# Kernel tuning notes

Hardware: AMD Instinct MI355X
Metric: run time of the kernel (lower is better)

## Reference

```python
import jax, jax.numpy as jnp
import numpy as np

EPS = 1e-6
NUM_HEADS = 16


def _layernorm(x, g, b):
    m = jnp.mean(x, axis=-1, keepdims=True)
    v = jnp.mean(jnp.square(x - m), axis=-1, keepdims=True)
    return (x - m) / jnp.sqrt(v + EPS) * g + b


def _rotate_half(x):
    x1, x2 = jnp.split(x, 2, axis=-1)
    return jnp.concatenate([-x2, x1], axis=-1)


def setup_inputs() -> dict:
    key = jax.random.key(0)
    B, N, C = 2, 2048, 1024
    H = NUM_HEADS
    D = C // H
    F = int(C * 4.0)
    ks = jax.random.split(key, 12)
    s = 0.02
    pos = jnp.arange(N)[:, None].astype(jnp.float32)
    inv_freq = 1.0 / (10000.0 ** (jnp.arange(0, D, 2, dtype=jnp.float32) / D))
    freqs = pos * inv_freq[None, :]          # [N, D/2]
    emb = jnp.concatenate([freqs, freqs], axis=-1)  # [N, D]
    return {
        "x": jax.random.normal(ks[0], (B, N, C), jnp.float32),
        "rotary_cos": jnp.cos(emb),
        "rotary_sin": jnp.sin(emb),
        "ln1_g": jnp.ones((C,), jnp.float32),
        "ln1_b": jnp.zeros((C,), jnp.float32),
        "Wq": jax.random.normal(ks[1], (C, C), jnp.float32) * s,
        "bq": jnp.zeros((C,), jnp.float32),
        "Wk": jax.random.normal(ks[2], (C, C), jnp.float32) * s,
        "bk": jnp.zeros((C,), jnp.float32),
        "Wv": jax.random.normal(ks[3], (C, C), jnp.float32) * s,
        "bv": jnp.zeros((C,), jnp.float32),
        "Wo": jax.random.normal(ks[4], (C, C), jnp.float32) * s,
        "bo": jnp.zeros((C,), jnp.float32),
        "ln2_g": jnp.ones((C,), jnp.float32),
        "ln2_b": jnp.zeros((C,), jnp.float32),
        "W1": jax.random.normal(ks[5], (F, C), jnp.float32) * s,
        "b1": jnp.zeros((F,), jnp.float32),
        "W2": jax.random.normal(ks[6], (C, F), jnp.float32) * s,
        "b2": jnp.zeros((C,), jnp.float32),
    }


def reference(x, rotary_cos, rotary_sin, ln1_g, ln1_b, Wq, bq, Wk, bk, Wv, bv,
              Wo, bo, ln2_g, ln2_b, W1, b1, W2, b2):
    B, N, C = x.shape
    H = NUM_HEADS
    D = C // H

    # --- attention branch ---
    h = _layernorm(x, ln1_g, ln1_b)
    q = (h @ Wq.T + bq).reshape(B, N, H, D).transpose(0, 2, 1, 3)  # [B,H,N,D]
    k = (h @ Wk.T + bk).reshape(B, N, H, D).transpose(0, 2, 1, 3)
    v = (h @ Wv.T + bv).reshape(B, N, H, D).transpose(0, 2, 1, 3)

    cos = rotary_cos[None, None, :, :]  # [1,1,N,D]
    sin = rotary_sin[None, None, :, :]
    q = q * cos + _rotate_half(q) * sin
    k = k * cos + _rotate_half(k) * sin

    scale = D ** -0.5
    attn = jnp.einsum('bhnd,bhmd->bhnm', q, k) * scale
    attn = jax.nn.softmax(attn, axis=-1)
    out = jnp.einsum('bhnm,bhmd->bhnd', attn, v)
    out = out.transpose(0, 2, 1, 3).reshape(B, N, C)
    out = out @ Wo.T + bo
    x = x + out

    # --- MLP branch ---
    h = _layernorm(x, ln2_g, ln2_b)
    h = jax.nn.gelu(h @ W1.T + b1, approximate=False)  # torch nn.GELU exact
    h = h @ W2.T + b2
    return x + h
```

## Files before the change

kernel.cpp:

```cpp
#include <hip/hip_runtime.h>
#include <hip/hip_bf16.h>

#define B_ 2
#define N_ 2048
#define C_ 1024
#define H_ 16
#define D_ 64
#define F_ 4096
#define M_ 4096

typedef __attribute__((ext_vector_type(8))) short bf16x8;
typedef __attribute__((ext_vector_type(4))) float f32x4;

__device__ inline unsigned short f2bf(float f) {
  unsigned int u = __float_as_uint(f);
  u = (u + 0x7FFFu + ((u >> 16) & 1u)) >> 16;
  return (unsigned short)u;
}

__global__ __launch_bounds__(256)
void cvt_all(const float4* __restrict__ s0, const float4* __restrict__ s1,
             const float4* __restrict__ s2, const float4* __restrict__ s3,
             const float4* __restrict__ s4, const float4* __restrict__ s5,
             ushort4* __restrict__ d0, ushort4* __restrict__ d1,
             ushort4* __restrict__ d2, ushort4* __restrict__ d3,
             ushort4* __restrict__ d4, ushort4* __restrict__ d5) {
  int b = blockIdx.x;
  const float4* s; ushort4* d; int i;
  if      (b < 1024) { s = s0; d = d0; i = b * 256 + threadIdx.x; }
  else if (b < 2048) { s = s1; d = d1; i = (b - 1024) * 256 + threadIdx.x; }
  else if (b < 3072) { s = s2; d = d2; i = (b - 2048) * 256 + threadIdx.x; }
  else if (b < 4096) { s = s3; d = d3; i = (b - 3072) * 256 + threadIdx.x; }
  else if (b < 8192) { s = s4; d = d4; i = (b - 4096) * 256 + threadIdx.x; }
  else               { s = s5; d = d5; i = (b - 8192) * 256 + threadIdx.x; }
  float4 f = s[i];
  ushort4 o;
  o.x = f2bf(f.x); o.y = f2bf(f.y); o.z = f2bf(f.z); o.w = f2bf(f.w);
  d[i] = o;
}

__global__ __launch_bounds__(256)
void ln_kernel(const float* __restrict__ x, const float* __restrict__ g,
               const float* __restrict__ b, unsigned short* __restrict__ out) {
  __shared__ float red[8];
  const int row = blockIdx.x;
  const int t = threadIdx.x;
  const float4 xv = *(const float4*)(x + row * 1024 + t * 4);
  float s  = xv.x + xv.y + xv.z + xv.w;
  float sq = xv.x * xv.x + xv.y * xv.y + xv.z * xv.z + xv.w * xv.w;
  #pragma unroll
  for (int off = 32; off >= 1; off >>= 1) {
    s  += __shfl_down(s, off);
    sq += __shfl_down(sq, off);
  }
  const int lane = t & 63, wave = t >> 6;
  if (lane == 0) { red[wave * 2] = s; red[wave * 2 + 1] = sq; }
  __syncthreads();
  float ts = red[0] + red[2] + red[4] + red[6];
  float tq = red[1] + red[3] + red[5] + red[7];
  float mean = ts * (1.0f / 1024.0f);
  float var  = tq * (1.0f / 1024.0f) - mean * mean;
  float rstd = rsqrtf(var + 1e-6f);
  float xs[4] = {xv.x, xv.y, xv.z, xv.w};
  #pragma unroll
  for (int i = 0; i < 4; i++) {
    int c = t * 4 + i;
    float y = (xs[i] - mean) * rstd * g[c] + b[c];
    out[row * 1024 + c] = f2bf(y);
  }
}

template<int MODE, int BN>
__global__ __launch_bounds__(256)
void gemm_bt(const unsigned short* __restrict__ A,
             const unsigned short* __restrict__ Bw,
             int K, int Nout, int npc,
             const float* __restrict__ bias,
             const float* __restrict__ resid,
             unsigned short* __restrict__ out_bf,
             float* __restrict__ out_f32) {
  constexpr int NJ = BN / 32;
  __shared__ unsigned short sA[2][128 * 64];
  __shared__ unsigned short sB[2][BN * 64];
  const int t = threadIdx.x;
  const int wave = t >> 6, lane = t & 63;
  const int quad = lane >> 4, l16 = lane & 15;
  const int wm = (wave & 1) * 64, wn = (wave >> 1) * (BN / 2);
  const int id = blockIdx.y * gridDim.x + blockIdx.x;
  const int xcd = id & 7, r_ = id >> 3;
  const int n_blk = xcd * npc + r_ % npc;
  const int m_blk = r_ / npc;
  const int m0 = m_blk * 128, n0 = n_blk * BN;

  f32x4 acc[4][NJ];
  #pragma unroll
  for (int i = 0; i < 4; i++)
    #pragma unroll
    for (int j = 0; j < NJ; j++) acc[i][j] = (f32x4){0.f, 0.f, 0.f, 0.f};

  const unsigned short* gA = A  + (m0 + (t >> 3)) * K + (t & 7) * 8;
  const unsigned short* gB = Bw + (n0 + (t >> 3)) * K + (t & 7) * 8;

  auto stage = [&](int k0, int buf) {
    unsigned short* lA = &sA[buf][(wave * 8) * 64];
    unsigned short* lB = &sB[buf][(wave * 8) * 64];
    #pragma unroll
    for (int i = 0; i < 4; i++)
      __builtin_amdgcn_global_load_lds((const unsigned int*)(gA + (32 * i) * K + k0),
                                       (unsigned int*)(lA + 32 * i * 64), 16, 0, 0);
    #pragma unroll
    for (int i = 0; i < BN / 32; i++)
      __builtin_amdgcn_global_load_lds((const unsigned int*)(gB + (32 * i) * K + k0),
                                       (unsigned int*)(lB + 32 * i * 64), 16, 0, 0);
  };

  stage(0, 0);
  __syncthreads();

  const int nk = K >> 6;
  for (int kt = 0; kt < nk; kt++) {
    const int cur = kt & 1;
    if (kt + 1 < nk) stage((kt + 1) * 64, cur ^ 1);
    #pragma unroll
    for (int kk = 0; kk < 2; kk++) {
      bf16x8 af[4], bfr[NJ];
      #pragma unroll
      for (int i = 0; i < 4; i++)
        af[i] = *(const bf16x8*)(&sA[cur][(wm + i * 16 + l16) * 64 + kk * 32 + quad * 8]);
      #pragma unroll
      for (int j = 0; j < NJ; j++)
        bfr[j] = *(const bf16x8*)(&sB[cur][(wn + j * 16 + l16) * 64 + kk * 32 + quad * 8]);
      #pragma unroll
      for (int i = 0; i < 4; i++)
        #pragma unroll
        for (int j = 0; j < NJ; j++)
          acc[i][j] = __builtin_amdgcn_mfma_f32_16x16x32_bf16(af[i], bfr[j], acc[i][j], 0, 0, 0);
    }
    __syncthreads();
  }

  #pragma unroll
  for (int i = 0; i < 4; i++) {
    #pragma unroll
    for (int j = 0; j < NJ; j++) {
      int col = n0 + wn + j * 16 + l16;
      #pragma unroll
      for (int r = 0; r < 4; r++) {
        int row = m0 + wm + i * 16 + quad * 4 + r;
        float v = acc[i][j][r];
        if (MODE == 1 || MODE == 3) {
          out_f32[row * Nout + col] = v + bias[col] + resid[row * Nout + col];
        } else {
          v += bias[col];
          float w = v * (1.0f + 0.044715f * v * v);
          float gl = v / (1.0f + __expf(-1.5957691216f * w));
          out_bf[row * Nout + col] = f2bf(gl);
        }
      }
    }
  }
}

__global__ __launch_bounds__(256)
void gemm_qkv(const unsigned short* __restrict__ A,
              const unsigned short* __restrict__ Bw,
              const float* __restrict__ bq, const float* __restrict__ bk,
              const float* __restrict__ bv,
              const float* __restrict__ rc, const float* __restrict__ rs,
              unsigned short* __restrict__ qo, unsigned short* __restrict__ ko,
              unsigned short* __restrict__ vt) {
  const int K = C_;
  __shared__ unsigned short sA[2][128 * 64];
  __shared__ unsigned short sB[2][128 * 64];
  const int t = threadIdx.x;
  const int wave = t >> 6, lane = t & 63;
  const int quad = lane >> 4, l16 = lane & 15;
  const int wm = (wave & 1) * 64, wn = (wave >> 1) * 64;
  const int id = blockIdx.y * gridDim.x + blockIdx.x;
  const int xcd = id & 7, r_ = id >> 3;
  const int n_blk = xcd * 3 + r_ % 3;
  const int m_blk = r_ / 3;
  const int m0 = m_blk * 128, n0 = n_blk * 128;

  f32x4 acc[4][4];
  #pragma unroll
  for (int i = 0; i < 4; i++)
    #pragma unroll
    for (int j = 0; j < 4; j++) acc[i][j] = (f32x4){0.f, 0.f, 0.f, 0.f};

  const unsigned short* gA = A  + (m0 + (t >> 3)) * K + (t & 7) * 8;
  const unsigned short* gB = Bw + (n0 + (t >> 3)) * K + (t & 7) * 8;

  auto stage = [&](int k0, int buf) {
    unsigned short* lA = &sA[buf][(wave * 8) * 64];
    unsigned short* lB = &sB[buf][(wave * 8) * 64];
    #pragma unroll
    for (int i = 0; i < 4; i++) {
      __builtin_amdgcn_global_load_lds((const unsigned int*)(gA + (32 * i) * K + k0),
                                       (unsigned int*)(lA + 32 * i * 64), 16, 0, 0);
      __builtin_amdgcn_global_load_lds((const unsigned int*)(gB + (32 * i) * K + k0),
                                       (unsigned int*)(lB + 32 * i * 64), 16, 0, 0);
    }
  };

  stage(0, 0);
  __syncthreads();

  const int nk = K >> 6;
  for (int kt = 0; kt < nk; kt++) {
    const int cur = kt & 1;
    if (kt + 1 < nk) stage((kt + 1) * 64, cur ^ 1);
    #pragma unroll
    for (int kk = 0; kk < 2; kk++) {
      bf16x8 af[4], bfr[4];
      #pragma unroll
      for (int i = 0; i < 4; i++)
        af[i] = *(const bf16x8*)(&sA[cur][(wm + i * 16 + l16) * 64 + kk * 32 + quad * 8]);
      #pragma unroll
      for (int j = 0; j < 4; j++)
        bfr[j] = *(const bf16x8*)(&sB[cur][(wn + j * 16 + l16) * 64 + kk * 32 + quad * 8]);
      #pragma unroll
      for (int i = 0; i < 4; i++)
        #pragma unroll
        for (int j = 0; j < 4; j++)
          acc[i][j] = __builtin_amdgcn_mfma_f32_16x16x32_bf16(af[i], bfr[j], acc[i][j], 0, 0, 0);
    }
    __syncthreads();
  }

  const int rgn = n_blk >> 3;
  const int c0 = (n_blk & 7) * 128;

  if (rgn == 2) {
    #pragma unroll
    for (int i = 0; i < 4; i++) {
      int row0 = m0 + wm + i * 16 + quad * 4;
      int bidx = row0 >> 11, n0r = row0 & 2047;
      #pragma unroll
      for (int j = 0; j < 4; j++) {
        int d = j * 16 + l16;
        int c = c0 + wn + d;
        int h = c >> 6;
        float bb = bv[c];
        __hip_bfloat162 p01 = __float22bfloat162_rn(float2{acc[i][j][0] + bb, acc[i][j][1] + bb});
        __hip_bfloat162 p23 = __float22bfloat162_rn(float2{acc[i][j][2] + bb, acc[i][j][3] + bb});
        unsigned int u01, u23;
        __builtin_memcpy(&u01, &p01, 4);
        __builtin_memcpy(&u23, &p23, 4);
        *(uint2*)(vt + (((bidx * 16 + h) * 64) + (c & 63)) * 2048 + n0r) = make_uint2(u01, u23);
      }
    }
  } else {
    const float* bias = (rgn == 0) ? bq : bk;
    unsigned short* outp = (rgn == 0) ? qo : ko;
    #pragma unroll
    for (int i = 0; i < 4; i++) {
      #pragma unroll
      for (int r = 0; r < 4; r++) {
        int row = m0 + wm + i * 16 + quad * 4 + r;
        int bidx = row >> 11, n = row & 2047;
        #pragma unroll
        for (int j = 0; j < 4; j++) {
          int d = j * 16 + l16;
          int c = c0 + wn + d;
          int h = c >> 6;
          int oi = ((bidx * 16 + h) * 2048 + n) * 64 + d;
          float val = acc[i][j][r] + bias[c];
          float pv  = acc[i][j ^ 2][r] + bias[c ^ 32];
          float rot = (j < 2) ? -pv : pv;
          float y = val * rc[n * 64 + d] + rot * rs[n * 64 + d];
          if (rgn == 0) y *= 0.125f;
          outp[oi] = f2bf(y);
        }
      }
    }
  }
}

__global__ __launch_bounds__(256)
void flash_attn(const unsigned short* __restrict__ q,
                const unsigned short* __restrict__ k,
                const unsigned short* __restrict__ vt,
                unsigned short* __restrict__ o) {
  __shared__ unsigned short sK[2][64 * 64];
  __shared__ unsigned short sVt[2][64 * 64];
  __shared__ unsigned short sPt[2][4][16 * 72];
  const int t = threadIdx.x;
  const int wave = t >> 6, lane = t & 63;
  const int quad = lane >> 4, l16 = lane & 15;
  const int id = blockIdx.y * gridDim.x + blockIdx.x;
  const int bh = (id & 7) * 4 + ((id >> 3) & 3);
  const int qb = id >> 5;
  const int base = bh * (N_ * D_);

  bf16x8 qa[2][2];
  #pragma unroll
  for (int qt = 0; qt < 2; qt++) {
    int qrow = qb * 128 + wave * 32 + qt * 16 + l16;
    #pragma unroll
    for (int kk = 0; kk < 2; kk++)
      qa[qt][kk] = *(const bf16x8*)(q + base + qrow * D_ + kk * 32 + quad * 8);
  }
  float l_i[2] = {0.f, 0.f};
  f32x4 o_acc[2][4];
  #pragma unroll
  for (int qt = 0; qt < 2; qt++)
    #pragma unroll
    for (int dt = 0; dt < 4; dt++) o_acc[qt][dt] = (f32x4){0.f, 0.f, 0.f, 0.f};

  const unsigned short* gK  = k  + base + (t >> 3) * 64 + (t & 7) * 8;
  const unsigned short* gVt = vt + bh * (64 * 2048) + (t >> 3) * 2048 + (t & 7) * 8;

  auto stage = [&](int kt, int buf) {
    unsigned short* lK = &sK[buf][(wave * 8) * 64];
    unsigned short* lV = &sVt[buf][(wave * 8) * 64];
    #pragma unroll
    for (int i = 0; i < 2; i++) {
      __builtin_amdgcn_global_load_lds((const unsigned int*)(gK + (kt * 64 + 32 * i) * 64),
                                       (unsigned int*)(lK + 32 * i * 64), 16, 0, 0);
      __builtin_amdgcn_global_load_lds((const unsigned int*)(gVt + 32 * i * 2048 + kt * 64),
                                       (unsigned int*)(lV + 32 * i * 64), 16, 0, 0);
    }
  };
  stage(0, 0);
  __syncthreads();

  for (int kt = 0; kt < N_ / 64; kt++) {
    const int cur = kt & 1;
    if (kt < N_ / 64 - 1) stage(kt + 1, cur ^ 1);

    f32x4 s_acc[2][4];
    #pragma unroll
    for (int nt = 0; nt < 4; nt++) {
      bf16x8 kb0 = *(const bf16x8*)(&sK[cur][(nt * 16 + l16) * 64 + quad * 8]);
      bf16x8 kb1 = *(const bf16x8*)(&sK[cur][(nt * 16 + l16) * 64 + 32 + quad * 8]);
      #pragma unroll
      for (int qt = 0; qt < 2; qt++) {
        f32x4 a = (f32x4){0.f, 0.f, 0.f, 0.f};
        a = __builtin_amdgcn_mfma_f32_16x16x32_bf16(kb0, qa[qt][0], a, 0, 0, 0);
        a = __builtin_amdgcn_mfma_f32_16x16x32_bf16(kb1, qa[qt][1], a, 0, 0, 0);
        s_acc[qt][nt] = a;
      }
    }
    #pragma unroll
    for (int qt = 0; qt < 2; qt++) {
      float rsum = 0.f;
      #pragma unroll
      for (int nt = 0; nt < 4; nt++)
        #pragma unroll
        for (int r = 0; r < 4; r++) {
          float p = __expf(s_acc[qt][nt][r]);
          s_acc[qt][nt][r] = p;
          rsum += p;
        }
      rsum += __shfl_xor(rsum, 16);
      rsum += __shfl_xor(rsum, 32);
      l_i[qt] += rsum;
      #pragma unroll
      for (int nt = 0; nt < 4; nt++) {
        __hip_bfloat162 p01 = __float22bfloat162_rn(float2{s_acc[qt][nt][0], s_acc[qt][nt][1]});
        __hip_bfloat162 p23 = __float22bfloat162_rn(float2{s_acc[qt][nt][2], s_acc[qt][nt][3]});
        unsigned int u01, u23;
        __builtin_memcpy(&u01, &p01, 4);
        __builtin_memcpy(&u23, &p23, 4);
        *(uint2*)(&sPt[qt][wave][l16 * 72 + nt * 16 + quad * 4]) = make_uint2(u01, u23);
      }
    }
    __asm__ volatile("s_waitcnt lgkmcnt(0)" ::: "memory");
    bf16x8 pt[2][2];
    #pragma unroll
    for (int qt = 0; qt < 2; qt++) {
      pt[qt][0] = *(const bf16x8*)(&sPt[qt][wave][l16 * 72 + quad * 8]);
      pt[qt][1] = *(const bf16x8*)(&sPt[qt][wave][l16 * 72 + 32 + quad * 8]);
    }
    #pragma unroll
    for (int dt = 0; dt < 4; dt++) {
      int d0 = dt * 16 + l16;
      bf16x8 va0 = *(const bf16x8*)(&sVt[cur][d0 * 64 + quad * 8]);
      bf16x8 va1 = *(const bf16x8*)(&sVt[cur][d0 * 64 + 32 + quad * 8]);
      #pragma unroll
      for (int qt = 0; qt < 2; qt++) {
        o_acc[qt][dt] = __builtin_amdgcn_mfma_f32_16x16x32_bf16(va0, pt[qt][0], o_acc[qt][dt], 0, 0, 0);
        o_acc[qt][dt] = __builtin_amdgcn_mfma_f32_16x16x32_bf16(va1, pt[qt][1], o_acc[qt][dt], 0, 0, 0);
      }
    }
    __syncthreads();
  }

  const int b = bh >> 4, h = bh & 15;
  #pragma unroll
  for (int qt = 0; qt < 2; qt++) {
    const float inv = 1.0f / l_i[qt];
    const int tok = b * N_ + qb * 128 + wave * 32 + qt * 16 + l16;
    #pragma unroll
    for (int dt = 0; dt < 4; dt++) {
      __hip_bfloat162 p01 = __float22bfloat162_rn(float2{o_acc[qt][dt][0] * inv, o_acc[qt][dt][1] * inv});
      __hip_bfloat162 p23 = __float22bfloat162_rn(float2{o_acc[qt][dt][2] * inv, o_acc[qt][dt][3] * inv});
      unsigned int u01, u23;
      __builtin_memcpy(&u01, &p01, 4);
      __builtin_memcpy(&u23, &p23, 4);
      int col = h * 64 + dt * 16 + quad * 4;
      *(uint2*)(o + tok * C_ + col) = make_uint2(u01, u23);
    }
  }
}

extern "C" void kernel_launch(void* const* d_in, const int* in_sizes, int n_in,
                              void* d_out, int out_size, void* d_ws, size_t ws_size,
                              hipStream_t stream) {
  const float* x   = (const float*)d_in[0];
  const float* rc  = (const float*)d_in[1];
  const float* rs  = (const float*)d_in[2];
  const float* g1  = (const float*)d_in[3];
  const float* be1 = (const float*)d_in[4];
  const float* Wq  = (const float*)d_in[5];
  const float* bq  = (const float*)d_in[6];
  const float* Wk  = (const float*)d_in[7];
  const float* bk  = (const float*)d_in[8];
  const float* Wv  = (const float*)d_in[9];
  const float* bv  = (const float*)d_in[10];
  const float* Wo  = (const float*)d_in[11];
  const float* bo  = (const float*)d_in[12];
  const float* g2  = (const float*)d_in[13];
  const float* be2 = (const float*)d_in[14];
  const float* W1  = (const float*)d_in[15];
  const float* b1m = (const float*)d_in[16];
  const float* W2  = (const float*)d_in[17];
  const float* b2m = (const float*)d_in[18];
  float* out = (float*)d_out;

  char* ws = (char*)d_ws;
  unsigned short* wqkv = (unsigned short*)(ws + 0);
  unsigned short* wo   = (unsigned short*)(ws + 6291456);
  unsigned short* w1   = (unsigned short*)(ws + 8388608);
  unsigned short* w2   = (unsigned short*)(ws + 16777216);
  unsigned short* h1   = (unsigned short*)(ws + 25165824);
  unsigned short* qa   = (unsigned short*)(ws + 33554432);
  unsigned short* ka   = (unsigned short*)(ws + 41943040);
  unsigned short* va   = (unsigned short*)(ws + 50331648);
  unsigned short* ao   = (unsigned short*)(ws + 58720256);
  float*          x1   = (float*)(ws + 67108864);
  unsigned short* u    = (unsigned short*)(ws + 33554432);

  cvt_all<<<12288, 256, 0, stream>>>(
      (const float4*)Wq, (const float4*)Wk, (const float4*)Wv, (const float4*)Wo,
      (const float4*)W1, (const float4*)W2,
      (ushort4*)wqkv, (ushort4*)(wqkv + 1048576), (ushort4*)(wqkv + 2097152),
      (ushort4*)wo, (ushort4*)w1, (ushort4*)w2);

  ln_kernel<<<4096, 256, 0, stream>>>(x, g1, be1, h1);
  gemm_qkv<<<dim3(24, 32), 256, 0, stream>>>(h1, wqkv, bq, bk, bv, rc, rs, qa, ka, va);
  flash_attn<<<dim3(16, 32), 256, 0, stream>>>(qa, ka, va, ao);
  gemm_bt<1, 64><<<dim3(16, 32), 256, 0, stream>>>(ao, wo, 1024, 1024, 2, bo, x, nullptr, x1);
  ln_kernel<<<4096, 256, 0, stream>>>(x1, g2, be2, h1);
  gemm_bt<2, 64><<<dim3(64, 32), 256, 0, stream>>>(h1, w1, 1024, 4096, 8, b1m, nullptr, u, nullptr);
  gemm_bt<3, 64><<<dim3(16, 32), 256, 0, stream>>>(u, w2, 4096, 1024, 2, b2m, x1, nullptr, out);
}
```

Measured before the change: 428.2 us.

## Add 256x256 pipelined GEMM for QKV/W1, XOR-swizzle LDS, remap block tiles

New measurement: 373.9 us. 1.15x faster.

```diff
diff --git a/kernel.cpp b/kernel.cpp
--- a/kernel.cpp
+++ b/kernel.cpp
@@ -88,8 +88,8 @@
   const int wm = (wave & 1) * 64, wn = (wave >> 1) * (BN / 2);
   const int id = blockIdx.y * gridDim.x + blockIdx.x;
   const int xcd = id & 7, r_ = id >> 3;
-  const int n_blk = xcd * npc + r_ % npc;
-  const int m_blk = r_ / npc;
+  const int m_blk = xcd * 4 + (r_ & 3);
+  const int n_blk = r_ >> 2;
   const int m0 = m_blk * 128, n0 = n_blk * BN;
 
   f32x4 acc[4][NJ];
@@ -98,8 +98,9 @@
     #pragma unroll
     for (int j = 0; j < NJ; j++) acc[i][j] = (f32x4){0.f, 0.f, 0.f, 0.f};
 
-  const unsigned short* gA = A  + (m0 + (t >> 3)) * K + (t & 7) * 8;
-  const unsigned short* gB = Bw + (n0 + (t >> 3)) * K + (t & 7) * 8;
+  const int sc = (((t & 7) ^ ((t >> 3) & 7)) * 8);
+  const unsigned short* gA = A  + (m0 + (t >> 3)) * K + sc;
+  const unsigned short* gB = Bw + (n0 + (t >> 3)) * K + sc;
 
   auto stage = [&](int k0, int buf) {
     unsigned short* lA = &sA[buf][(wave * 8) * 64];
@@ -117,19 +118,23 @@
   stage(0, 0);
   __syncthreads();
 
+  const int so0 = ((quad ^ (l16 & 7)) * 8);
+  const int so1 = (((4 + quad) ^ (l16 & 7)) * 8);
+
   const int nk = K >> 6;
   for (int kt = 0; kt < nk; kt++) {
     const int cur = kt & 1;
     if (kt + 1 < nk) stage((kt + 1) * 64, cur ^ 1);
     #pragma unroll
     for (int kk = 0; kk < 2; kk++) {
+      const int so = kk ? so1 : so0;
       bf16x8 af[4], bfr[NJ];
       #pragma unroll
       for (int i = 0; i < 4; i++)
-        af[i] = *(const bf16x8*)(&sA[cur][(wm + i * 16 + l16) * 64 + kk * 32 + quad * 8]);
+        af[i] = *(const bf16x8*)(&sA[cur][(wm + i * 16 + l16) * 64 + so]);
       #pragma unroll
       for (int j = 0; j < NJ; j++)
-        bfr[j] = *(const bf16x8*)(&sB[cur][(wn + j * 16 + l16) * 64 + kk * 32 + quad * 8]);
+        bfr[j] = *(const bf16x8*)(&sB[cur][(wn + j * 16 + l16) * 64 + so]);
       #pragma unroll
       for (int i = 0; i < 4; i++)
         #pragma unroll
@@ -161,116 +166,166 @@
   }
 }
 
-__global__ __launch_bounds__(256)
-void gemm_qkv(const unsigned short* __restrict__ A,
-              const unsigned short* __restrict__ Bw,
-              const float* __restrict__ bq, const float* __restrict__ bk,
-              const float* __restrict__ bv,
-              const float* __restrict__ rc, const float* __restrict__ rs,
-              unsigned short* __restrict__ qo, unsigned short* __restrict__ ko,
-              unsigned short* __restrict__ vt) {
-  const int K = C_;
-  __shared__ unsigned short sA[2][128 * 64];
-  __shared__ unsigned short sB[2][128 * 64];
+template<int EPI>
+__global__ __launch_bounds__(512, 1)
+void gemm256(const unsigned short* __restrict__ A,
+             const unsigned short* __restrict__ Bw,
+             const float* __restrict__ bias,
+             const float* __restrict__ bq, const float* __restrict__ bk,
+             const float* __restrict__ bv,
+             const float* __restrict__ rc, const float* __restrict__ rs,
+             unsigned short* __restrict__ o0,
+             unsigned short* __restrict__ ko, unsigned short* __restrict__ vt) {
+  const int K = 1024;
+  __shared__ unsigned short sA[2][256 * 64];
+  __shared__ unsigned short sB[2][256 * 64];
   const int t = threadIdx.x;
   const int wave = t >> 6, lane = t & 63;
   const int quad = lane >> 4, l16 = lane & 15;
-  const int wm = (wave & 1) * 64, wn = (wave >> 1) * 64;
-  const int id = blockIdx.y * gridDim.x + blockIdx.x;
+  const int wm = (wave & 1) * 128, wn = (wave >> 1) * 64;
+  const int id = blockIdx.x;
   const int xcd = id & 7, r_ = id >> 3;
-  const int n_blk = xcd * 3 + r_ % 3;
-  const int m_blk = r_ / 3;
-  const int m0 = m_blk * 128, n0 = n_blk * 128;
-
-  f32x4 acc[4][4];
-  #pragma unroll
-  for (int i = 0; i < 4; i++)
+  int m_blk, n_blk;
+  if (EPI == 0) { n_blk = xcd * 2 + (r_ >> 4); m_blk = r_ & 15; }
+  else          { m_blk = xcd * 2 + r_ / 12;   n_blk = r_ % 12; }
+  const int m0 = m_blk * 256, n0 = n_blk * 256;
+
+  f32x4 acc[8][4];
+  #pragma unroll
+  for (int i = 0; i < 8; i++)
     #pragma unroll
     for (int j = 0; j < 4; j++) acc[i][j] = (f32x4){0.f, 0.f, 0.f, 0.f};
 
-  const unsigned short* gA = A  + (m0 + (t >> 3)) * K + (t & 7) * 8;
-  const unsigned short* gB = Bw + (n0 + (t >> 3)) * K + (t & 7) * 8;
-
-  auto stage = [&](int k0, int buf) {
-    unsigned short* lA = &sA[buf][(wave * 8) * 64];
-    unsigned short* lB = &sB[buf][(wave * 8) * 64];
-    #pragma unroll
-    for (int i = 0; i < 4; i++) {
-      __builtin_amdgcn_global_load_lds((const unsigned int*)(gA + (32 * i) * K + k0),
-                                       (unsigned int*)(lA + 32 * i * 64), 16, 0, 0);
-      __builtin_amdgcn_global_load_lds((const unsigned int*)(gB + (32 * i) * K + k0),
-                                       (unsigned int*)(lB + 32 * i * 64), 16, 0, 0);
+  const int sc = (((t & 7) ^ ((t >> 3) & 7)) * 8);
+  const unsigned short* gA = A  + (m0 + (t >> 3)) * K + sc;
+  const unsigned short* gB = Bw + (n0 + (t >> 3)) * K + sc;
+
+  auto stage_pair = [&](int k0, int buf, int pr) {
+    if (pr < 2) {
+      unsigned short* lA = &sA[buf][(wave * 8) * 64];
+      #pragma unroll
+      for (int r = pr * 2; r < pr * 2 + 2; r++)
+        __builtin_amdgcn_global_load_lds((const unsigned int*)(gA + (64 * r) * K + k0),
+                                         (unsigned int*)(lA + 64 * r * 64), 16, 0, 0);
+    } else {
+      unsigned short* lB = &sB[buf][(wave * 8) * 64];
+      #pragma unroll
+      for (int r = (pr - 2) * 2; r < (pr - 2) * 2 + 2; r++)
+        __builtin_amdgcn_global_load_lds((const unsigned int*)(gB + (64 * r) * K + k0),
+                                         (unsigned int*)(lB + 64 * r * 64), 16, 0, 0);
     }
   };
 
-  stage(0, 0);
-  __syncthreads();
+  stage_pair(0, 0, 0); stage_pair(0, 0, 1); stage_pair(0, 0, 2); stage_pair(0, 0, 3);
+  stage_pair(64, 1, 0);
+  asm volatile("s_waitcnt vmcnt(2)" ::: "memory");
+  __builtin_amdgcn_s_barrier();
+
+  const int so0 = ((quad ^ (l16 & 7)) * 8);
+  const int so1 = (((4 + quad) ^ (l16 & 7)) * 8);
 
   const int nk = K >> 6;
-  for (int kt = 0; kt < nk; kt++) {
-    const int cur = kt & 1;
-    if (kt + 1 < nk) stage((kt + 1) * 64, cur ^ 1);
-    #pragma unroll
-    for (int kk = 0; kk < 2; kk++) {
+  for (int t_ = 0; t_ < nk; t_++) {
+    const int R = t_ & 1;
+    const unsigned short* rA = sA[R];
+    const unsigned short* rB = sB[R];
+    #pragma unroll
+    for (int p = 0; p < 4; p++) {
+      const int kk = p >> 1, ih = p & 1;
+      const int so = kk ? so1 : so0;
       bf16x8 af[4], bfr[4];
       #pragma unroll
-      for (int i = 0; i < 4; i++)
-        af[i] = *(const bf16x8*)(&sA[cur][(wm + i * 16 + l16) * 64 + kk * 32 + quad * 8]);
+      for (int ii = 0; ii < 4; ii++)
+        af[ii] = *(const bf16x8*)(&rA[(wm + (ih * 4 + ii) * 16 + l16) * 64 + so]);
       #pragma unroll
       for (int j = 0; j < 4; j++)
-        bfr[j] = *(const bf16x8*)(&sB[cur][(wn + j * 16 + l16) * 64 + kk * 32 + quad * 8]);
-      #pragma unroll
-      for (int i = 0; i < 4; i++)
+        bfr[j] = *(const bf16x8*)(&rB[(wn + j * 16 + l16) * 64 + so]);
+      if (p < 3 && t_ + 1 < nk) stage_pair((t_ + 1) * 64, R ^ 1, p + 1);
+      __builtin_amdgcn_s_barrier();
+      asm volatile("s_waitcnt lgkmcnt(0)" ::: "memory");
+      __builtin_amdgcn_sched_barrier(0);
+      __builtin_amdgcn_s_setprio(1);
+      #pragma unroll
+      for (int ii = 0; ii < 4; ii++)
         #pragma unroll
         for (int j = 0; j < 4; j++)
-          acc[i][j] = __builtin_amdgcn_mfma_f32_16x16x32_bf16(af[i], bfr[j], acc[i][j], 0, 0, 0);
-    }
-    __syncthreads();
-  }
-
-  const int rgn = n_blk >> 3;
-  const int c0 = (n_blk & 7) * 128;
-
-  if (rgn == 2) {
-    #pragma unroll
-    for (int i = 0; i < 4; i++) {
-      int row0 = m0 + wm + i * 16 + quad * 4;
-      int bidx = row0 >> 11, n0r = row0 & 2047;
+          acc[ih * 4 + ii][j] =
+              __builtin_amdgcn_mfma_f32_16x16x32_bf16(af[ii], bfr[j], acc[ih * 4 + ii][j], 0, 0, 0);
+      __builtin_amdgcn_s_setprio(0);
+      if (p < 3) __builtin_amdgcn_s_barrier();
+    }
+    __builtin_amdgcn_s_barrier();
+    if (t_ + 2 < nk) {
+      stage_pair((t_ + 2) * 64, R, 0);
+      asm volatile("s_waitcnt vmcnt(2)" ::: "memory");
+      __builtin_amdgcn_s_barrier();
+    } else if (t_ + 1 < nk) {
+      asm volatile("s_waitcnt vmcnt(0)" ::: "memory");
+      __builtin_amdgcn_s_barrier();
+    }
+  }
+
+  if (EPI == 0) {
+    #pragma unroll
+    for (int i = 0; i < 8; i++) {
       #pragma unroll
       for (int j = 0; j < 4; j++) {
-        int d = j * 16 + l16;
-        int c = c0 + wn + d;
-        int h = c >> 6;
-        float bb = bv[c];
-        __hip_bfloat162 p01 = __float22bfloat162_rn(float2{acc[i][j][0] + bb, acc[i][j][1] + bb});
-        __hip_bfloat162 p23 = __float22bfloat162_rn(float2{acc[i][j][2] + bb, acc[i][j][3] + bb});
-        unsigned int u01, u23;
-        __builtin_memcpy(&u01, &p01, 4);
-        __builtin_memcpy(&u23, &p23, 4);
-        *(uint2*)(vt + (((bidx * 16 + h) * 64) + (c & 63)) * 2048 + n0r) = make_uint2(u01, u23);
+        int col = n0 + wn + j * 16 + l16;
+        float bb = bias[col];
+        #pragma unroll
+        for (int r = 0; r < 4; r++) {
+          int row = m0 + wm + i * 16 + quad * 4 + r;
+          float v = acc[i][j][r] + bb;
+          float w = v * (1.0f + 0.044715f * v * v);
+          float gl = v / (1.0f + __expf(-1.5957691216f * w));
+          o0[row * 4096 + col] = f2bf(gl);
+        }
       }
     }
   } else {
-    const float* bias = (rgn == 0) ? bq : bk;
-    unsigned short* outp = (rgn == 0) ? qo : ko;
-    #pragma unroll
-    for (int i = 0; i < 4; i++) {
-      #pragma unroll
-      for (int r = 0; r < 4; r++) {
-        int row = m0 + wm + i * 16 + quad * 4 + r;
-        int bidx = row >> 11, n = row & 2047;
+    const int rgn = n_blk >> 2;
+    const int c0 = (n_blk & 3) * 256;
+    if (rgn == 2) {
+      #pragma unroll
+      for (int i = 0; i < 8; i++) {
+        int row0 = m0 + wm + i * 16 + quad * 4;
+        int bidx = row0 >> 11, n0r = row0 & 2047;
         #pragma unroll
         for (int j = 0; j < 4; j++) {
           int d = j * 16 + l16;
           int c = c0 + wn + d;
           int h = c >> 6;
-          int oi = ((bidx * 16 + h) * 2048 + n) * 64 + d;
-          float val = acc[i][j][r] + bias[c];
-          float pv  = acc[i][j ^ 2][r] + bias[c ^ 32];
-          float rot = (j < 2) ? -pv : pv;
-          float y = val * rc[n * 64 + d] + rot * rs[n * 64 + d];
-          if (rgn == 0) y *= 0.125f;
-          outp[oi] = f2bf(y);
+          float bb = bv[c];
+          __hip_bfloat162 p01 = __float22bfloat162_rn(float2{acc[i][j][0] + bb, acc[i][j][1] + bb});
+          __hip_bfloat162 p23 = __float22bfloat162_rn(float2{acc[i][j][2] + bb, acc[i][j][3] + bb});
+          unsigned int u01, u23;
+          __builtin_memcpy(&u01, &p01, 4);
+          __builtin_memcpy(&u23, &p23, 4);
+          *(uint2*)(vt + (((bidx * 16 + h) * 64) + d) * 2048 + n0r) = make_uint2(u01, u23);
+        }
+      }
+    } else {
+      const float* bia = (rgn == 0) ? bq : bk;
+      unsigned short* outp = (rgn == 0) ? o0 : ko;
+      #pragma unroll
+      for (int i = 0; i < 8; i++) {
+        #pragma unroll
+        for (int r = 0; r < 4; r++) {
+          int row = m0 + wm + i * 16 + quad * 4 + r;
+          int bidx = row >> 11, n = row & 2047;
+          #pragma unroll
+          for (int j = 0; j < 4; j++) {
+            int d = j * 16 + l16;
+            int c = c0 + wn + d;
+            int h = c >> 6;
+            int oi = ((bidx * 16 + h) * 2048 + n) * 64 + d;
+            float val = acc[i][j][r] + bia[c];
+            float pv  = acc[i][j ^ 2][r] + bia[c ^ 32];
+            float rot = (j < 2) ? -pv : pv;
+            float y = val * rc[n * 64 + d] + rot * rs[n * 64 + d];
+            if (rgn == 0) y *= 0.125f;
+            outp[oi] = f2bf(y);
+          }
         }
       }
     }
@@ -308,8 +363,9 @@
     #pragma unroll
     for (int dt = 0; dt < 4; dt++) o_acc[qt][dt] = (f32x4){0.f, 0.f, 0.f, 0.f};
 
-  const unsigned short* gK  = k  + base + (t >> 3) * 64 + (t & 7) * 8;
-  const unsigned short* gVt = vt + bh * (64 * 2048) + (t >> 3) * 2048 + (t & 7) * 8;
+  const int sc = (((t & 7) ^ ((t >> 3) & 7)) * 8);
+  const unsigned short* gK  = k  + base + (t >> 3) * 64 + sc;
+  const unsigned short* gVt = vt + bh * (64 * 2048) + (t >> 3) * 2048 + sc;
 
   auto stage = [&](int kt, int buf) {
     unsigned short* lK = &sK[buf][(wave * 8) * 64];
@@ -325,6 +381,9 @@
   stage(0, 0);
   __syncthreads();
 
+  const int so0 = ((quad ^ (l16 & 7)) * 8);
+  const int so1 = (((4 + quad) ^ (l16 & 7)) * 8);
+
   for (int kt = 0; kt < N_ / 64; kt++) {
     const int cur = kt & 1;
     if (kt < N_ / 64 - 1) stage(kt + 1, cur ^ 1);
@@ -332,8 +391,8 @@
     f32x4 s_acc[2][4];
     #pragma unroll
     for (int nt = 0; nt < 4; nt++) {
-      bf16x8 kb0 = *(const bf16x8*)(&sK[cur][(nt * 16 + l16) * 64 + quad * 8]);
-      bf16x8 kb1 = *(const bf16x8*)(&sK[cur][(nt * 16 + l16) * 64 + 32 + quad * 8]);
+      bf16x8 kb0 = *(const bf16x8*)(&sK[cur][(nt * 16 + l16) * 64 + so0]);
+      bf16x8 kb1 = *(const bf16x8*)(&sK[cur][(nt * 16 + l16) * 64 + so1]);
       #pragma unroll
       for (int qt = 0; qt < 2; qt++) {
         f32x4 a = (f32x4){0.f, 0.f, 0.f, 0.f};
@@ -376,8 +435,8 @@
     #pragma unroll
     for (int dt = 0; dt < 4; dt++) {
       int d0 = dt * 16 + l16;
-      bf16x8 va0 = *(const bf16x8*)(&sVt[cur][d0 * 64 + quad * 8]);
-      bf16x8 va1 = *(const bf16x8*)(&sVt[cur][d0 * 64 + 32 + quad * 8]);
+      bf16x8 va0 = *(const bf16x8*)(&sVt[cur][d0 * 64 + so0]);
+      bf16x8 va1 = *(const bf16x8*)(&sVt[cur][d0 * 64 + so1]);
       #pragma unroll
       for (int qt = 0; qt < 2; qt++) {
         o_acc[qt][dt] = __builtin_amdgcn_mfma_f32_16x16x32_bf16(va0, pt[qt][0], o_acc[qt][dt], 0, 0, 0);
@@ -449,10 +508,11 @@
       (ushort4*)wo, (ushort4*)w1, (ushort4*)w2);
 
   ln_kernel<<<4096, 256, 0, stream>>>(x, g1, be1, h1);
-  gemm_qkv<<<dim3(24, 32), 256, 0, stream>>>(h1, wqkv, bq, bk, bv, rc, rs, qa, ka, va);
+  gemm256<1><<<192, 512, 0, stream>>>(h1, wqkv, nullptr, bq, bk, bv, rc, rs, qa, ka, va);
   flash_attn<<<dim3(16, 32), 256, 0, stream>>>(qa, ka, va, ao);
   gemm_bt<1, 64><<<dim3(16, 32), 256, 0, stream>>>(ao, wo, 1024, 1024, 2, bo, x, nullptr, x1);
   ln_kernel<<<4096, 256, 0, stream>>>(x1, g2, be2, h1);
-  gemm_bt<2, 64><<<dim3(64, 32), 256, 0, stream>>>(h1, w1, 1024, 4096, 8, b1m, nullptr, u, nullptr);
+  gemm256<0><<<256, 512, 0, stream>>>(h1, w1, b1m, nullptr, nullptr, nullptr, nullptr, nullptr,
+                                      u, nullptr, nullptr);
   gemm_bt<3, 64><<<dim3(16, 32), 256, 0, stream>>>(u, w2, 4096, 1024, 2, b2m, x1, nullptr, out);
 }
```
